# Performance work log

Measured on AMD Instinct MI355X. Metric: run time of the kernel, lower is better.

Reference implementation:

```python
import jax, jax.numpy as jnp
import numpy as np

DIM = 4096
N_HEADS = 32
HEAD_DIM = DIM // N_HEADS  # 128
SEQ = 2048
BATCH = 2


def _rope_freqs(seq_len, head_dim, theta=10000.0):
    inv = 1.0 / (theta ** (np.arange(0, head_dim, 2, dtype=np.float32) / head_dim))
    ang = np.outer(np.arange(seq_len, dtype=np.float32), inv)  # [S, hd/2]
    return jnp.asarray(np.cos(ang)), jnp.asarray(np.sin(ang))


def setup_inputs() -> dict:
    key = jax.random.key(0)
    ks = jax.random.split(key, 10)
    s = 1.0 / np.sqrt(DIM)
    inp = {
        "x": jax.random.normal(ks[0], (BATCH, SEQ, DIM), dtype=jnp.float32),
        "wq_w": jax.random.normal(ks[1], (DIM, DIM), dtype=jnp.float32) * s,
        "wq_b": jax.random.normal(ks[2], (DIM,), dtype=jnp.float32) * 0.01,
        "wk_w": jax.random.normal(ks[3], (DIM, DIM), dtype=jnp.float32) * s,
        "wk_b": jax.random.normal(ks[4], (DIM,), dtype=jnp.float32) * 0.01,
        "wv_w": jax.random.normal(ks[5], (DIM, DIM), dtype=jnp.float32) * s,
        "wv_b": jax.random.normal(ks[6], (DIM,), dtype=jnp.float32) * 0.01,
        "wo_w": jax.random.normal(ks[7], (DIM, DIM), dtype=jnp.float32) * s,
        "wo_b": jax.random.normal(ks[8], (DIM,), dtype=jnp.float32) * 0.01,
    }
    cos, sin = _rope_freqs(SEQ, HEAD_DIM)
    inp["freqs_cos"] = cos  # [S, hd/2]
    inp["freqs_sin"] = sin
    return inp


def _apply_rope(x, cos, sin):
    # x: [B, S, H, D]; cos/sin: [S, D/2] -> broadcast [1, S, 1, D/2]
    B, S, H, D = x.shape
    xr = x.reshape(B, S, H, D // 2, 2)
    re, im = xr[..., 0], xr[..., 1]
    c = cos[None, :, None, :]
    s = sin[None, :, None, :]
    out_re = re * c - im * s
    out_im = re * s + im * c
    return jnp.stack([out_re, out_im], axis=-1).reshape(B, S, H, D)


def reference(x, freqs_cos, freqs_sin, wq_w, wq_b, wk_w, wk_b, wv_w, wv_b, wo_w, wo_b):
    B, S, C = x.shape
    H, D = N_HEADS, HEAD_DIM
    xq = (x @ wq_w.T + wq_b).reshape(B, S, H, D)
    xk = (x @ wk_w.T + wk_b).reshape(B, S, H, D)
    xv = (x @ wv_w.T + wv_b).reshape(B, S, H, D)
    xq = _apply_rope(xq, freqs_cos, freqs_sin)
    xk = _apply_rope(xk, freqs_cos, freqs_sin)
    # [B, H, S, D]
    xq = xq.transpose(0, 2, 1, 3)
    xk = xk.transpose(0, 2, 1, 3)
    xv = xv.transpose(0, 2, 1, 3)
    scale = 1.0 / jnp.sqrt(jnp.asarray(D, dtype=x.dtype))
    scores = jnp.einsum('bhsd,bhtd->bhst', xq, xk) * scale
    causal = jnp.tril(jnp.ones((S, S), dtype=bool))
    scores = jnp.where(causal[None, None], scores, jnp.asarray(-jnp.inf, dtype=scores.dtype))
    attn = jax.nn.softmax(scores, axis=-1)
    y = jnp.einsum('bhst,bhtd->bhsd', attn, xv)  # [B, H, S, D]
    # faithful to source: transpose(-1,-2) then view(B, S, -1) -> raw reshape of [B,H,D,S]
    y = y.transpose(0, 1, 3, 2).reshape(B, S, H * D)
    return y @ wo_w.T + wo_b
```

## Files before the change

### kernel.cpp

```cpp
#include <hip/hip_runtime.h>
#include <hip/hip_bf16.h>

typedef __hip_bfloat16 bf16;
typedef short s16x8 __attribute__((ext_vector_type(8)));
typedef float fx4 __attribute__((ext_vector_type(4)));
typedef unsigned int u32;

#define DIM 4096
#define SEQ 2048
#define NH 32
#define HD 128

#define MFMA_BF16(a,b,c) __builtin_amdgcn_mfma_f32_16x16x32_bf16((a),(b),(c),0,0,0)

__device__ __forceinline__ void gload16(const bf16* g, const bf16* l) {
  __builtin_amdgcn_global_load_lds((const __attribute__((address_space(1))) u32*)g,
                                   (__attribute__((address_space(3))) u32*)l, 16, 0, 0);
}

__global__ void cvt_f32_bf16(const float* __restrict__ in, bf16* __restrict__ out, int n8)
{
  int i = blockIdx.x * blockDim.x + threadIdx.x;
  const int stride = gridDim.x * blockDim.x;
  for (; i < n8; i += stride) {
    fx4 a = ((const fx4*)in)[2 * i], b = ((const fx4*)in)[2 * i + 1];
    s16x8 o; bf16* op = (bf16*)&o;
    #pragma unroll
    for (int j = 0; j < 4; ++j) { op[j] = __float2bfloat16(a[j]); op[4 + j] = __float2bfloat16(b[j]); }
    ((s16x8*)out)[i] = o;
  }
}

__global__ __launch_bounds__(512, 1)
void gemm256(const bf16* __restrict__ A, const bf16* __restrict__ W,
             const float* __restrict__ bias,
             const float* __restrict__ fcos, const float* __restrict__ fsin,
             void* __restrict__ outv, int mode)
{
  __shared__ __align__(16) bf16 As[2][256 * 64];
  __shared__ __align__(16) bf16 Bs[2][256 * 64];
  const int tid = threadIdx.x;
  const int wid = tid >> 6;
  const int lane = tid & 63;
  const int l15 = lane & 15, lg = lane >> 4;
  const int wm = wid >> 2, wn = wid & 3;
  const int brow = blockIdx.y * 256, bcol = blockIdx.x * 256;
  const int rsub = lane >> 3;
  const int scol = ((lane & 7) ^ rsub) * 8;

  fx4 acc[8][4] = {};

  #pragma unroll
  for (int tt = 0; tt < 2; ++tt) {
    #pragma unroll
    for (int j = 0; j < 4; ++j) {
      const int chunk = j * 8 + wid;
      const int row = chunk * 8 + rsub;
      gload16(A + (size_t)(brow + row) * DIM + tt * 64 + scol, &As[tt][chunk * 512]);
      gload16(W + (size_t)(bcol + row) * DIM + tt * 64 + scol, &Bs[tt][chunk * 512]);
    }
  }

  for (int t = 0; t < 64; ++t) {
    const int p = t & 1;
    if (t < 63) asm volatile("s_waitcnt vmcnt(8)" ::: "memory");
    else        asm volatile("s_waitcnt vmcnt(0)" ::: "memory");
    __builtin_amdgcn_s_barrier();
    __builtin_amdgcn_sched_barrier(0);

    s16x8 afr[2][8], bfr[2][4];
    #pragma unroll
    for (int kk = 0; kk < 2; ++kk) {
      #pragma unroll
      for (int mi = 0; mi < 8; ++mi) {
        const int r = wm * 128 + mi * 16 + l15;
        afr[kk][mi] = *(const s16x8*)&As[p][r * 64 + ((((kk * 4 + lg)) ^ (r & 7)) << 3)];
      }
      #pragma unroll
      for (int nj = 0; nj < 4; ++nj) {
        const int r = wn * 64 + nj * 16 + l15;
        bfr[kk][nj] = *(const s16x8*)&Bs[p][r * 64 + ((((kk * 4 + lg)) ^ (r & 7)) << 3)];
      }
    }
    asm volatile("s_waitcnt lgkmcnt(0)" ::: "memory");
    __builtin_amdgcn_sched_barrier(0);
    __builtin_amdgcn_s_barrier();
    __builtin_amdgcn_sched_barrier(0);

    if (t + 2 < 64) {
      const int k0 = (t + 2) * 64;
      #pragma unroll
      for (int j = 0; j < 4; ++j) {
        const int chunk = j * 8 + wid;
        const int row = chunk * 8 + rsub;
        gload16(A + (size_t)(brow + row) * DIM + k0 + scol, &As[p][chunk * 512]);
        gload16(W + (size_t)(bcol + row) * DIM + k0 + scol, &Bs[p][chunk * 512]);
      }
    }

    __builtin_amdgcn_s_setprio(1);
    #pragma unroll
    for (int kk = 0; kk < 2; ++kk)
      #pragma unroll
      for (int mi = 0; mi < 8; ++mi)
        #pragma unroll
        for (int nj = 0; nj < 4; ++nj)
          acc[mi][nj] = MFMA_BF16(afr[kk][mi], bfr[kk][nj], acc[mi][nj]);
    __builtin_amdgcn_s_setprio(0);
  }

  #pragma unroll
  for (int mi = 0; mi < 8; ++mi) {
    const int mbase = brow + wm * 128 + mi * 16 + lg * 4;
    #pragma unroll
    for (int nj = 0; nj < 4; ++nj) {
      const int n = bcol + wn * 64 + nj * 16 + l15;
      const float bv = bias[n];
      #pragma unroll
      for (int r = 0; r < 4; ++r) {
        const int m = mbase + r;
        float val = acc[mi][nj][r] + bv;
        if (mode <= 1) {
          const float pv = __shfl_xor(val, 1);
          const int sp = m & (SEQ - 1);
          const int fi = (n >> 1) & 63;
          const float c = fcos[sp * 64 + fi];
          const float s = fsin[sp * 64 + fi];
          val = (n & 1) ? (pv * s + val * c) : (val * c - pv * s);
        }
        if (mode == 3) {
          ((float*)outv)[(size_t)m * DIM + n] = val;
        } else {
          const int b = m >> 11, sp = m & (SEQ - 1);
          const int h = n >> 7, d = n & (HD - 1);
          ((bf16*)outv)[((size_t)(b * NH + h) * SEQ + sp) * HD + d] = __float2bfloat16(val);
        }
      }
    }
  }
}

__global__ __launch_bounds__(256, 2)
void gemm_slow(const void* __restrict__ Av, const float* __restrict__ Wf,
               const float* __restrict__ bias,
               const float* __restrict__ fcos, const float* __restrict__ fsin,
               void* __restrict__ outv, int mode)
{
  __shared__ __align__(16) bf16 As[128 * 64];
  __shared__ __align__(16) bf16 Bs[128 * 64];
  const int abf = (mode == 3) ? 1 : 0;
  const int tid = threadIdx.x;
  const int wid = tid >> 6;
  const int lane = tid & 63;
  const int l15 = lane & 15, lg = lane >> 4;
  const int wr = wid >> 1, wc = wid & 1;
  const int brow = blockIdx.y * 128, bcol = blockIdx.x * 128;

  fx4 acc[4][4] = {};

  for (int k0 = 0; k0 < DIM; k0 += 64) {
    #pragma unroll
    for (int i = 0; i < 4; ++i) {
      const int v = i * 256 + tid;
      const int row = v >> 3;
      const int c8 = (v & 7) * 8;
      s16x8 a, b;
      if (abf) {
        a = *(const s16x8*)&((const bf16*)Av)[(size_t)(brow + row) * DIM + k0 + c8];
      } else {
        const float* Af = (const float*)Av;
        fx4 a0 = *(const fx4*)&Af[(size_t)(brow + row) * DIM + k0 + c8];
        fx4 a1 = *(const fx4*)&Af[(size_t)(brow + row) * DIM + k0 + c8 + 4];
        bf16* ap = (bf16*)&a;
        #pragma unroll
        for (int j = 0; j < 4; ++j) { ap[j] = __float2bfloat16(a0[j]); ap[4 + j] = __float2bfloat16(a1[j]); }
      }
      {
        fx4 b0 = *(const fx4*)&Wf[(size_t)(bcol + row) * DIM + k0 + c8];
        fx4 b1 = *(const fx4*)&Wf[(size_t)(bcol + row) * DIM + k0 + c8 + 4];
        bf16* bp = (bf16*)&b;
        #pragma unroll
        for (int j = 0; j < 4; ++j) { bp[j] = __float2bfloat16(b0[j]); bp[4 + j] = __float2bfloat16(b1[j]); }
      }
      *(s16x8*)&As[row * 64 + c8] = a;
      *(s16x8*)&Bs[row * 64 + c8] = b;
    }
    __syncthreads();
    #pragma unroll
    for (int kk = 0; kk < 2; ++kk) {
      s16x8 af[4], bfr[4];
      #pragma unroll
      for (int mi = 0; mi < 4; ++mi)
        af[mi] = *(const s16x8*)&As[(wr * 64 + mi * 16 + l15) * 64 + kk * 32 + lg * 8];
      #pragma unroll
      for (int nj = 0; nj < 4; ++nj)
        bfr[nj] = *(const s16x8*)&Bs[(wc * 64 + nj * 16 + l15) * 64 + kk * 32 + lg * 8];
      #pragma unroll
      for (int mi = 0; mi < 4; ++mi)
        #pragma unroll
        for (int nj = 0; nj < 4; ++nj)
          acc[mi][nj] = MFMA_BF16(af[mi], bfr[nj], acc[mi][nj]);
    }
    __syncthreads();
  }

  #pragma unroll
  for (int mi = 0; mi < 4; ++mi) {
    const int mbase = brow + wr * 64 + mi * 16 + lg * 4;
    #pragma unroll
    for (int nj = 0; nj < 4; ++nj) {
      const int n = bcol + wc * 64 + nj * 16 + l15;
      const float bv = bias[n];
      #pragma unroll
      for (int r = 0; r < 4; ++r) {
        const int m = mbase + r;
        float val = acc[mi][nj][r] + bv;
        if (mode <= 1) {
          const float pv = __shfl_xor(val, 1);
          const int sp = m & (SEQ - 1);
          const int fi = (n >> 1) & 63;
          const float c = fcos[sp * 64 + fi];
          const float s = fsin[sp * 64 + fi];
          val = (n & 1) ? (pv * s + val * c) : (val * c - pv * s);
        }
        if (mode == 3) {
          ((float*)outv)[(size_t)m * DIM + n] = val;
        } else {
          const int b = m >> 11, sp = m & (SEQ - 1);
          const int h = n >> 7, d = n & (HD - 1);
          ((bf16*)outv)[((size_t)(b * NH + h) * SEQ + sp) * HD + d] = __float2bfloat16(val);
        }
      }
    }
  }
}

#define SOFTMAX_PHASE(sa, o, mrun, lrun, q0)                                   \
  {                                                                            \
    _Pragma("unroll")                                                          \
    for (int r = 0; r < 4; ++r) {                                              \
      const int q = (q0) + lg * 4 + r;                                         \
      float mx = -__builtin_inff();                                            \
      _Pragma("unroll")                                                        \
      for (int nj = 0; nj < 4; ++nj) {                                         \
        float v = sa[nj][r] * scale;                                           \
        if (diagM && (t0 + nj * 16 + l15 > q)) v = -__builtin_inff();          \
        sa[nj][r] = v;                                                         \
        mx = fmaxf(mx, v);                                                     \
      }                                                                        \
      _Pragma("unroll")                                                        \
      for (int off = 1; off < 16; off <<= 1) mx = fmaxf(mx, __shfl_xor(mx, off)); \
      const float mnew = fmaxf(mrun[r], mx);                                   \
      const float fsc = __expf(mrun[r] - mnew);                                \
      mrun[r] = mnew;                                                          \
      float rs = 0.f;                                                          \
      _Pragma("unroll")                                                        \
      for (int nj = 0; nj < 4; ++nj) {                                         \
        const float pp = __expf(sa[nj][r] - mnew);                             \
        sa[nj][r] = pp;                                                        \
        rs += pp;                                                              \
      }                                                                        \
      _Pragma("unroll")                                                        \
      for (int off = 1; off < 16; off <<= 1) rs += __shfl_xor(rs, off);        \
      lrun[r] = lrun[r] * fsc + rs;                                            \
      _Pragma("unroll")                                                        \
      for (int dj = 0; dj < 8; ++dj) o[dj][r] *= fsc;                          \
    }                                                                          \
  }

__global__ __launch_bounds__(256, 2)
void attn_fwd(const bf16* __restrict__ Q, const bf16* __restrict__ K,
              const bf16* __restrict__ V, bf16* __restrict__ ymat)
{
  __shared__ __align__(16) bf16 smem[32768];
  bf16* Kl   = smem;
  bf16* Vrow = smem + 8192;
  bf16* Vt   = smem + 16384;
  bf16* PlA  = smem + 24576;
  bf16* PlB  = smem + 28672;
  bf16* Ys   = smem;

  const int tid = threadIdx.x, wid = tid >> 6, lane = tid & 63;
  const int l15 = lane & 15, lg = lane >> 4;
  const int pair = blockIdx.x, bh = blockIdx.y;
  const int qtA = pair, qtB = 31 - pair;
  const int b = bh >> 5, h = bh & 31;
  const bf16* Qb = Q + (size_t)bh * SEQ * HD;
  const bf16* Kb = K + (size_t)bh * SEQ * HD;
  const bf16* Vb = V + (size_t)bh * SEQ * HD;
  const int q0A = qtA * 64 + wid * 16;
  const int q0B = qtB * 64 + wid * 16;

  s16x8 aqA[4], aqB[4];
  #pragma unroll
  for (int kk = 0; kk < 4; ++kk) {
    aqA[kk] = *(const s16x8*)&Qb[(size_t)(q0A + l15) * HD + kk * 32 + lg * 8];
    aqB[kk] = *(const s16x8*)&Qb[(size_t)(q0B + l15) * HD + kk * 32 + lg * 8];
  }

  fx4 oA[8] = {}, oB[8] = {};
  float mA[4], lA[4], mB[4], lB[4];
  #pragma unroll
  for (int r = 0; r < 4; ++r) {
    mA[r] = -__builtin_inff(); lA[r] = 0.f;
    mB[r] = -__builtin_inff(); lB[r] = 0.f;
  }
  const float scale = 0.08838834764831845f;

  for (int kt = 0; kt <= qtB; ++kt) {
    const int t0 = kt * 64;
    const bool doA = (kt <= qtA);

    #pragma unroll
    for (int i = 0; i < 4; ++i) {
      const int chunk = i * 4 + wid;
      const int row = chunk * 4 + lg;
      const int col = ((l15 ^ (row & 7)) * 8);
      gload16(Kb + (size_t)(t0 + row) * HD + col, Kl + chunk * 512);
      gload16(Vb + (size_t)(t0 + row) * HD + col, Vrow + chunk * 512);
    }
    __syncthreads();

    fx4 sA[4], sB[4];
    #pragma unroll
    for (int nj = 0; nj < 4; ++nj) {
      fx4 sa = {}, sb = {};
      #pragma unroll
      for (int kk = 0; kk < 4; ++kk) {
        const int trow = nj * 16 + l15;
        const int colp = (kk * 32 + lg * 8) ^ ((trow & 7) << 3);
        s16x8 bk = *(const s16x8*)&Kl[trow * HD + colp];
        sb = MFMA_BF16(aqB[kk], bk, sb);
        if (doA) sa = MFMA_BF16(aqA[kk], bk, sa);
      }
      sB[nj] = sb; sA[nj] = sa;
    }

    #pragma unroll
    for (int it = 0; it < 2; ++it) {
      const int p = lane;
      const int tg = it * 4 + wid;
      s16x8 lo, hi; bf16* lop = (bf16*)&lo; bf16* hip = (bf16*)&hi;
      #pragma unroll
      for (int j = 0; j < 8; ++j) {
        const int t = tg * 8 + j;
        const u32 v32 = *(const u32*)((const char*)Vrow + t * 256 + ((p * 4) ^ (j << 4)));
        lop[j] = ((const bf16*)&v32)[0];
        hip[j] = ((const bf16*)&v32)[1];
      }
      *(s16x8*)((char*)Vt + (2 * p) * 128 + ((tg * 16) ^ ((p & 7) << 4))) = lo;
      *(s16x8*)((char*)Vt + (2 * p + 1) * 128 + ((tg * 16) ^ ((p & 7) << 4))) = hi;
    }

    {
      const bool diagM = (kt == qtB);
      SOFTMAX_PHASE(sB, oB, mB, lB, q0B)
      #pragma unroll
      for (int r = 0; r < 4; ++r) {
        const int row = lg * 4 + r;
        #pragma unroll
        for (int nj = 0; nj < 4; ++nj) {
          const int colp = (nj * 16 + l15) ^ ((row & 7) << 3);
          PlB[wid * 1024 + row * 64 + colp] = __float2bfloat16(sB[nj][r]);
        }
      }
    }
    if (doA) {
      const bool diagM = (kt == qtA);
      SOFTMAX_PHASE(sA, oA, mA, lA, q0A)
      #pragma unroll
      for (int r = 0; r < 4; ++r) {
        const int row = lg * 4 + r;
        #pragma unroll
        for (int nj = 0; nj < 4; ++nj) {
          const int colp = (nj * 16 + l15) ^ ((row & 7) << 3);
          PlA[wid * 1024 + row * 64 + colp] = __float2bfloat16(sA[nj][r]);
        }
      }
    }
    __syncthreads();

    s16x8 paA[2], paB[2];
    #pragma unroll
    for (int k2 = 0; k2 < 2; ++k2) {
      const int colp = (k2 * 32 + lg * 8) ^ ((l15 & 7) << 3);
      paB[k2] = *(const s16x8*)&PlB[wid * 1024 + l15 * 64 + colp];
      if (doA) paA[k2] = *(const s16x8*)&PlA[wid * 1024 + l15 * 64 + colp];
    }
    #pragma unroll
    for (int dj = 0; dj < 8; ++dj) {
      const int d = dj * 16 + l15;
      #pragma unroll
      for (int k2 = 0; k2 < 2; ++k2) {
        const int colp = (k2 * 32 + lg * 8) ^ (((d >> 1) & 7) << 3);
        s16x8 bv = *(const s16x8*)&Vt[d * 64 + colp];
        oB[dj] = MFMA_BF16(paB[k2], bv, oB[dj]);
        if (doA) oA[dj] = MFMA_BF16(paA[k2], bv, oA[dj]);
      }
    }
    __syncthreads();
  }

  #pragma unroll
  for (int dj = 0; dj < 8; ++dj) {
    const int d = dj * 16 + l15;
    const int lr = d >> 1;
    const int cbase = (d & 1) * 128 + wid * 16 + lg * 4;
    const int sw = (lr & 7) << 3;
    #pragma unroll
    for (int r = 0; r < 4; ++r) {
      Ys[lr * 256 + ((cbase + r) ^ sw)]       = __float2bfloat16(oA[dj][r] / lA[r]);
      Ys[lr * 256 + ((cbase + 64 + r) ^ sw)]  = __float2bfloat16(oB[dj][r] / lB[r]);
    }
  }
  __syncthreads();

  const size_t growbase = (size_t)(b * SEQ + h * 64) * DIM;
  #pragma unroll
  for (int it = 0; it < 8; ++it) {
    const int f = it * 256 + tid;
    const int lr = f >> 5;
    const int cu = f & 31;
    s16x8 v = *(const s16x8*)&Ys[lr * 256 + ((cu ^ (lr & 7)) << 3)];
    const int seg = cu >> 3;
    const int off = (cu & 7) * 8;
    const int par = seg >> 1, ab = seg & 1;
    const int qbase = (ab ? qtB : qtA) * 64;
    *(s16x8*)&ymat[growbase + (size_t)lr * DIM + par * 2048 + qbase + off] = v;
  }
}

extern "C" void kernel_launch(void* const* d_in, const int* in_sizes, int n_in,
                              void* d_out, int out_size, void* d_ws, size_t ws_size,
                              hipStream_t stream)
{
  (void)in_sizes; (void)n_in; (void)out_size;
  const float* x  = (const float*)d_in[0];
  const float* wq = (const float*)d_in[1];
  const float* bq = (const float*)d_in[2];
  const float* wk = (const float*)d_in[3];
  const float* bk = (const float*)d_in[4];
  const float* wv = (const float*)d_in[5];
  const float* bv = (const float*)d_in[6];
  const float* wo = (const float*)d_in[7];
  const float* bo = (const float*)d_in[8];
  const float* fc = (const float*)d_in[9];
  const float* fs = (const float*)d_in[10];

  const size_t NE = (size_t)2 * SEQ * DIM;
  const size_t NW = (size_t)DIM * DIM;
  const size_t SLOT = NE * sizeof(bf16);
  const size_t NEED_FAST = 6 * SLOT + 256;
  const size_t NEED_SLOW = 4 * SLOT + 256;

  dim3 blk(256);
  if (ws_size >= NEED_FAST) {
    bf16* xb = (bf16*)((char*)d_ws + 256);
    bf16* wb = xb + NE;
    bf16* qb = wb + NW;
    bf16* kb = qb + NE;
    bf16* vb = kb + NE;
    bf16* ym = vb + NE;
    const int n8x = (int)(NE / 8), n8w = (int)(NW / 8);
    dim3 cg(2048);
    dim3 blk2(512), gg2(16, 16);
    hipLaunchKernelGGL(cvt_f32_bf16, cg, blk, 0, stream, x, xb, n8x);
    hipLaunchKernelGGL(cvt_f32_bf16, cg, blk, 0, stream, wq, wb, n8w);
    hipLaunchKernelGGL(gemm256, gg2, blk2, 0, stream, xb, wb, bq, fc, fs, qb, 0);
    hipLaunchKernelGGL(cvt_f32_bf16, cg, blk, 0, stream, wk, wb, n8w);
    hipLaunchKernelGGL(gemm256, gg2, blk2, 0, stream, xb, wb, bk, fc, fs, kb, 1);
    hipLaunchKernelGGL(cvt_f32_bf16, cg, blk, 0, stream, wv, wb, n8w);
    hipLaunchKernelGGL(gemm256, gg2, blk2, 0, stream, xb, wb, bv, fc, fs, vb, 2);
    hipLaunchKernelGGL(attn_fwd, dim3(16, 64), blk, 0, stream, qb, kb, vb, ym);
    hipLaunchKernelGGL(cvt_f32_bf16, cg, blk, 0, stream, wo, wb, n8w);
    hipLaunchKernelGGL(gemm256, gg2, blk2, 0, stream, ym, wb, bo, fc, fs, d_out, 3);
  } else if (ws_size >= NEED_SLOW) {
    bf16* qb = (bf16*)((char*)d_ws + 256);
    bf16* kb = qb + NE;
    bf16* vb = kb + NE;
    bf16* ym = vb + NE;
    dim3 gg(32, 32);
    hipLaunchKernelGGL(gemm_slow, gg, blk, 0, stream, x, wq, bq, fc, fs, qb, 0);
    hipLaunchKernelGGL(gemm_slow, gg, blk, 0, stream, x, wk, bk, fc, fs, kb, 1);
    hipLaunchKernelGGL(gemm_slow, gg, blk, 0, stream, x, wv, bv, fc, fs, vb, 2);
    hipLaunchKernelGGL(attn_fwd, dim3(16, 64), blk, 0, stream, qb, kb, vb, ym);
    hipLaunchKernelGGL(gemm_slow, gg, blk, 0, stream, ym, wo, bo, fc, fs, d_out, 3);
  }
}
```

Before: 867.5 us.

## Reuse K smem for per-wave P tiles, raise attention occupancy, split GEMM MFMA phases

The attention kernel drops its separate PlA/PlB buffers and writes each wave's probability tile into the now-dead K tile region. This cuts LDS from 64KB to 48KB so launch bounds can ask for three blocks per CU. A barrier is added after the V transpose, and the P·V MFMAs for tiles B and A now run right after each softmax instead of after a shared sync. In the projection GEMM, the first k-slice MFMAs are issued before the LDS wait/barrier, so they overlap the remaining fragment loads. The tighter register budget at three blocks per CU risks spills.

```diff
diff --git a/kernel.cpp b/kernel.cpp
--- a/kernel.cpp
+++ b/kernel.cpp
@@ -82,6 +82,15 @@
         bfr[kk][nj] = *(const s16x8*)&Bs[p][r * 64 + ((((kk * 4 + lg)) ^ (r & 7)) << 3)];
       }
     }
+
+    __builtin_amdgcn_s_setprio(1);
+    #pragma unroll
+    for (int mi = 0; mi < 8; ++mi)
+      #pragma unroll
+      for (int nj = 0; nj < 4; ++nj)
+        acc[mi][nj] = MFMA_BF16(afr[0][mi], bfr[0][nj], acc[mi][nj]);
+    __builtin_amdgcn_s_setprio(0);
+
     asm volatile("s_waitcnt lgkmcnt(0)" ::: "memory");
     __builtin_amdgcn_sched_barrier(0);
     __builtin_amdgcn_s_barrier();
@@ -100,12 +109,10 @@
 
     __builtin_amdgcn_s_setprio(1);
     #pragma unroll
-    for (int kk = 0; kk < 2; ++kk)
-      #pragma unroll
-      for (int mi = 0; mi < 8; ++mi)
-        #pragma unroll
-        for (int nj = 0; nj < 4; ++nj)
-          acc[mi][nj] = MFMA_BF16(afr[kk][mi], bfr[kk][nj], acc[mi][nj]);
+    for (int mi = 0; mi < 8; ++mi)
+      #pragma unroll
+      for (int nj = 0; nj < 4; ++nj)
+        acc[mi][nj] = MFMA_BF16(afr[1][mi], bfr[1][nj], acc[mi][nj]);
     __builtin_amdgcn_s_setprio(0);
   }
 
@@ -268,20 +275,20 @@
     }                                                                          \
   }
 
-__global__ __launch_bounds__(256, 2)
+__global__ __launch_bounds__(256, 3)
 void attn_fwd(const bf16* __restrict__ Q, const bf16* __restrict__ K,
               const bf16* __restrict__ V, bf16* __restrict__ ymat)
 {
-  __shared__ __align__(16) bf16 smem[32768];
+  __shared__ __align__(16) bf16 smem[24576];
   bf16* Kl   = smem;
   bf16* Vrow = smem + 8192;
   bf16* Vt   = smem + 16384;
-  bf16* PlA  = smem + 24576;
-  bf16* PlB  = smem + 28672;
   bf16* Ys   = smem;
 
   const int tid = threadIdx.x, wid = tid >> 6, lane = tid & 63;
   const int l15 = lane & 15, lg = lane >> 4;
+  bf16* Pl = Kl + wid * 1024;
+
   const int pair = blockIdx.x, bh = blockIdx.y;
   const int qtA = pair, qtB = 31 - pair;
   const int b = bh >> 5, h = bh & 31;
@@ -351,6 +358,7 @@
       *(s16x8*)((char*)Vt + (2 * p) * 128 + ((tg * 16) ^ ((p & 7) << 4))) = lo;
       *(s16x8*)((char*)Vt + (2 * p + 1) * 128 + ((tg * 16) ^ ((p & 7) << 4))) = hi;
     }
+    __syncthreads();
 
     {
       const bool diagM = (kt == qtB);
@@ -361,7 +369,23 @@
         #pragma unroll
         for (int nj = 0; nj < 4; ++nj) {
           const int colp = (nj * 16 + l15) ^ ((row & 7) << 3);
-          PlB[wid * 1024 + row * 64 + colp] = __float2bfloat16(sB[nj][r]);
+          Pl[row * 64 + colp] = __float2bfloat16(sB[nj][r]);
+        }
+      }
+      s16x8 pa[2];
+      #pragma unroll
+      for (int k2 = 0; k2 < 2; ++k2) {
+        const int colp = (k2 * 32 + lg * 8) ^ ((l15 & 7) << 3);
+        pa[k2] = *(const s16x8*)&Pl[l15 * 64 + colp];
+      }
+      #pragma unroll
+      for (int dj = 0; dj < 8; ++dj) {
+        const int d = dj * 16 + l15;
+        #pragma unroll
+        for (int k2 = 0; k2 < 2; ++k2) {
+          const int colp = (k2 * 32 + lg * 8) ^ (((d >> 1) & 7) << 3);
+          s16x8 bv = *(const s16x8*)&Vt[d * 64 + colp];
+          oB[dj] = MFMA_BF16(pa[k2], bv, oB[dj]);
         }
       }
     }
@@ -374,28 +398,24 @@
         #pragma unroll
         for (int nj = 0; nj < 4; ++nj) {
           const int colp = (nj * 16 + l15) ^ ((row & 7) << 3);
-          PlA[wid * 1024 + row * 64 + colp] = __float2bfloat16(sA[nj][r]);
-        }
-      }
-    }
-    __syncthreads();
-
-    s16x8 paA[2], paB[2];
-    #pragma unroll
-    for (int k2 = 0; k2 < 2; ++k2) {
-      const int colp = (k2 * 32 + lg * 8) ^ ((l15 & 7) << 3);
-      paB[k2] = *(const s16x8*)&PlB[wid * 1024 + l15 * 64 + colp];
-      if (doA) paA[k2] = *(const s16x8*)&PlA[wid * 1024 + l15 * 64 + colp];
-    }
-    #pragma unroll
-    for (int dj = 0; dj < 8; ++dj) {
-      const int d = dj * 16 + l15;
+          Pl[row * 64 + colp] = __float2bfloat16(sA[nj][r]);
+        }
+      }
+      s16x8 pa[2];
       #pragma unroll
       for (int k2 = 0; k2 < 2; ++k2) {
-        const int colp = (k2 * 32 + lg * 8) ^ (((d >> 1) & 7) << 3);
-        s16x8 bv = *(const s16x8*)&Vt[d * 64 + colp];
-        oB[dj] = MFMA_BF16(paB[k2], bv, oB[dj]);
-        if (doA) oA[dj] = MFMA_BF16(paA[k2], bv, oA[dj]);
+        const int colp = (k2 * 32 + lg * 8) ^ ((l15 & 7) << 3);
+        pa[k2] = *(const s16x8*)&Pl[l15 * 64 + colp];
+      }
+      #pragma unroll
+      for (int dj = 0; dj < 8; ++dj) {
+        const int d = dj * 16 + l15;
+        #pragma unroll
+        for (int k2 = 0; k2 < 2; ++k2) {
+          const int colp = (k2 * 32 + lg * 8) ^ (((d >> 1) & 7) << 3);
+          s16x8 bv = *(const s16x8*)&Vt[d * 64 + colp];
+          oA[dj] = MFMA_BF16(pa[k2], bv, oA[dj]);
+        }
       }
     }
     __syncthreads();
```

New measurement: 1.127 ms. 29.9% more time.
